# Kernel optimization log

Measured on AMD Instinct MI355X. Metric: run time of the kernel, lower is better.

## Reference

```python
import jax, jax.numpy as jnp
import numpy as np

EMBED_DIM = 1024
NUM_HEADS = 16
HEAD_DIM = EMBED_DIM // NUM_HEADS  # 64
B, T = 4, 2048
ROPE_BASE = 10000.0


def rope_tables(T, head_dim):
    # matches RotaryPositionalEmbedding: inv_freq over even indices
    inv_freq = 1.0 / (ROPE_BASE ** (jnp.arange(0, head_dim, 2, dtype=jnp.float32) / head_dim))
    freqs = jnp.arange(T, dtype=jnp.float32)[:, None] * inv_freq[None, :]  # [T, head_dim//2]
    emb = jnp.concatenate([freqs, freqs], axis=-1)  # [T, head_dim]
    return jnp.cos(emb), jnp.sin(emb)


def apply_rotary(x, cos, sin):
    # x: [B, H, T, D]; cos/sin: [T, D] but only first D//2 cols used (as in torch code)
    d = x.shape[-1] // 2
    x1, x2 = x[..., :d], x[..., d:]
    c = cos[None, None, :, :d]
    s = sin[None, None, :, :d]
    return jnp.concatenate([x1 * c - x2 * s, x1 * s + x2 * c], axis=-1)


def setup_inputs() -> dict:
    key = jax.random.key(0)
    k1, k2, k3, k4 = jax.random.split(key, 4)
    x = jax.random.normal(k1, (B, T, EMBED_DIM), dtype=jnp.float32)
    attention_mask = jnp.ones((B, T), dtype=jnp.int32)
    W_qkv = jax.random.normal(k2, (EMBED_DIM, 3 * EMBED_DIM), dtype=jnp.float32) / np.sqrt(EMBED_DIM)
    W_out = jax.random.normal(k3, (EMBED_DIM, EMBED_DIM), dtype=jnp.float32) / np.sqrt(EMBED_DIM)
    b_out = jax.random.normal(k4, (EMBED_DIM,), dtype=jnp.float32) * 0.01
    return {"x": x, "attention_mask": attention_mask, "W_qkv": W_qkv, "W_out": W_out, "b_out": b_out}


def reference(x, attention_mask, W_qkv, W_out, b_out):
    Bq, Tq, C = x.shape
    H, D = NUM_HEADS, HEAD_DIM
    qkv = (x @ W_qkv).reshape(Bq, Tq, 3, H, D)
    qkv = jnp.transpose(qkv, (2, 0, 3, 1, 4))  # [3, B, H, T, D]
    q, k, v = qkv[0], qkv[1], qkv[2]

    cos, sin = rope_tables(Tq, D)
    q = apply_rotary(q, cos, sin)
    k = apply_rotary(k, cos, sin)

    scale = 1.0 / np.sqrt(D)
    attn = jnp.einsum('bhtd,bhsd->bhts', q, k) * scale  # [B, H, T, T]
    causal = jnp.tril(jnp.ones((Tq, Tq), dtype=bool))
    attn = jnp.where(causal[None, None], attn, -jnp.inf)
    pad = attention_mask[:, None, None, :] != 0  # [B,1,1,T]
    attn = jnp.where(pad, attn, -jnp.inf)
    attn = jax.nn.softmax(attn, axis=-1)
    out = jnp.einsum('bhts,bhsd->bthd', attn, v).reshape(Bq, Tq, C)
    return out @ W_out + b_out
```

## Files before the change

### kernel.cpp

```cpp
#include <hip/hip_runtime.h>
#include <hip/hip_bf16.h>
#include <math.h>

typedef __attribute__((ext_vector_type(8))) __bf16 bf16x8;
typedef __attribute__((ext_vector_type(4))) __bf16 bf16x4;
typedef __attribute__((ext_vector_type(4))) float f32x4;

#define B_ 4
#define T_ 2048
#define C_ 1024
#define H_ 16
#define D_ 64
#define M_TOT (B_*T_)

static __device__ __forceinline__ f32x4 mfma_bf16(bf16x8 a, bf16x8 b, f32x4 c) {
  return __builtin_amdgcn_mfma_f32_16x16x32_bf16(a, b, c, 0, 0, 0);
}

static __device__ __forceinline__ void gload_lds16(const void* g, void* l) {
  __builtin_amdgcn_global_load_lds((const __attribute__((address_space(1))) void*)g,
                                   (__attribute__((address_space(3))) void*)l, 16, 0, 0);
}

__global__ void prep_cvt_rope(const float* __restrict__ in, __bf16* __restrict__ out,
                              float* __restrict__ cosT, float* __restrict__ sinT) {
  const int bid = blockIdx.x;
  if (bid < 8192) {
    int i = bid * 256 + threadIdx.x;
    float4 v = ((const float4*)in)[i];
    bf16x4 o = { (__bf16)v.x, (__bf16)v.y, (__bf16)v.z, (__bf16)v.w };
    *(bf16x4*)(out + (size_t)i*4) = o;
  } else {
    int idx = (bid - 8192) * 256 + threadIdx.x;
    int t = idx >> 5, d = idx & 31;
    float inv = powf(10000.0f, -((float)(2*d)) / 64.0f);
    float ang = (float)t * inv;
    cosT[idx] = cosf(ang);
    sinT[idx] = sinf(ang);
  }
}

__global__ void prep_transpose(const float* __restrict__ Wqkv, __bf16* __restrict__ wqkvT,
                               const float* __restrict__ Wout, __bf16* __restrict__ woutT) {
  __shared__ float tile[32][33];
  const int bx = blockIdx.x;
  const float* in;  __bf16* out;  int N, n0;
  if (bx < 96) { in = Wqkv; out = wqkvT; N = 3072; n0 = bx * 32; }
  else         { in = Wout; out = woutT; N = 1024; n0 = (bx - 96) * 32; }
  const int K = 1024;
  int k0 = blockIdx.y * 32;
  int tx = threadIdx.x & 31, ty = threadIdx.x >> 5;
  #pragma unroll
  for (int r = ty; r < 32; r += 8) tile[r][tx] = in[(size_t)(k0 + r)*N + n0 + tx];
  __syncthreads();
  #pragma unroll
  for (int r = ty; r < 32; r += 8) out[(size_t)(n0 + r)*K + k0 + tx] = (__bf16)tile[tx][r];
}

__global__ void __launch_bounds__(256)
vtrans_k(const __bf16* __restrict__ v, __bf16* __restrict__ vt) {
  __shared__ __bf16 tile[64][72];
  const int tid = threadIdx.x;
  const int bh = blockIdx.y;
  const int t0 = blockIdx.x * 64;
  const __bf16* src = v + ((size_t)bh*T_ + t0)*D_;
  #pragma unroll
  for (int c = 0; c < 2; ++c) {
    int idx = tid + c*256;
    int row = idx >> 3, col8 = (idx & 7) * 8;
    *(bf16x8*)&tile[row][col8] = *(const bf16x8*)(src + row*D_ + col8);
  }
  __syncthreads();
  __bf16* dst = vt + (size_t)bh*D_*T_ + t0;
  #pragma unroll
  for (int c = 0; c < 2; ++c) {
    int idx = tid + c*256;
    int d = idx >> 3, t8 = (idx & 7) * 8;
    bf16x8 ov;
    #pragma unroll
    for (int j = 0; j < 8; ++j) ov[j] = tile[t8 + j][d];
    *(bf16x8*)(dst + (size_t)d*T_ + t8) = ov;
  }
}


#define GEMM_PHASES(N_TILES)                                                     \
  auto RD_BFR = [&](const char* lb, bf16x8 (*bfr)[2]) {                          \
    _Pragma("unroll")                                                            \
    for (int n = 0; n < 4; ++n) {                                                \
      const int row = wc*64 + n*16 + l15;                                        \
      const int sw = (row & 7) << 4;                                             \
      _Pragma("unroll")                                                          \
      for (int ks = 0; ks < 2; ++ks)                                             \
        bfr[n][ks] = *(const bf16x8*)(lb + row*128 + ((ks*64 + lhi*16) ^ sw));   \
    }                                                                            \
  };                                                                             \
  auto RD_AF = [&](const char* la, int mb, bf16x8 (*af)[2]) {                    \
    _Pragma("unroll")                                                            \
    for (int mm = 0; mm < 2; ++mm) {                                             \
      const int row = wr*64 + (mb + mm)*16 + l15;                                \
      const int sw = (row & 7) << 4;                                             \
      _Pragma("unroll")                                                          \
      for (int ks = 0; ks < 2; ++ks)                                             \
        af[mm][ks] = *(const bf16x8*)(la + row*128 + ((ks*64 + lhi*16) ^ sw));   \
    }                                                                            \
  };                                                                             \
  auto MFMA16 = [&](bf16x8 (*af)[2], bf16x8 (*bfr)[2], int mb) {                 \
    __builtin_amdgcn_s_setprio(1);                                               \
    _Pragma("unroll")                                                            \
    for (int mm = 0; mm < 2; ++mm)                                               \
      _Pragma("unroll")                                                          \
      for (int n = 0; n < 4; ++n)                                                \
        _Pragma("unroll")                                                        \
        for (int ks = 0; ks < 2; ++ks)                                           \
          acc[mb + mm][n] = mfma_bf16(af[mm][ks], bfr[n][ks], acc[mb + mm][n]);  \
    __builtin_amdgcn_s_setprio(0);                                               \
  };                                                                             \
  STAGE_B(0, (char*)lB[0]); STAGE_A(0, (char*)lA[0]); STAGE_B(1, (char*)lB[1]);  \
  asm volatile("s_waitcnt vmcnt(4)" ::: "memory");                               \
  __builtin_amdgcn_s_barrier();                                                  \
  _Pragma("unroll")                                                              \
  for (int it = 0; it < (N_TILES)/2; ++it) {                                     \
    const int t0 = it*2;                                                         \
    bf16x8 bfr[4][2], af[2][2];                                                  \
    RD_BFR((const char*)lB[0], bfr);                                             \
    RD_AF((const char*)lA[0], 0, af);                                            \
    STAGE_A(t0 + 1, (char*)lA[1]);                                               \
    __builtin_amdgcn_s_barrier();                                                \
    MFMA16(af, bfr, 0);                                                          \
    __builtin_amdgcn_s_barrier();                                                \
    RD_AF((const char*)lA[0], 2, af);                                            \
    if (t0 + 2 < (N_TILES)) STAGE_B(t0 + 2, (char*)lB[0]);                       \
    __builtin_amdgcn_s_barrier();                                                \
    MFMA16(af, bfr, 2);                                                          \
    if (t0 + 2 < (N_TILES)) asm volatile("s_waitcnt vmcnt(4)" ::: "memory");     \
    else                    asm volatile("s_waitcnt vmcnt(0)" ::: "memory");     \
    __builtin_amdgcn_s_barrier();                                                \
    RD_BFR((const char*)lB[1], bfr);                                             \
    RD_AF((const char*)lA[1], 0, af);                                            \
    if (t0 + 2 < (N_TILES)) STAGE_A(t0 + 2, (char*)lA[0]);                       \
    __builtin_amdgcn_s_barrier();                                                \
    MFMA16(af, bfr, 0);                                                          \
    __builtin_amdgcn_s_barrier();                                                \
    RD_AF((const char*)lA[1], 2, af);                                            \
    if (t0 + 3 < (N_TILES)) STAGE_B(t0 + 3, (char*)lB[1]);                       \
    __builtin_amdgcn_s_barrier();                                                \
    MFMA16(af, bfr, 2);                                                          \
    if (it < (N_TILES)/2 - 1) asm volatile("s_waitcnt vmcnt(4)" ::: "memory");   \
    __builtin_amdgcn_s_barrier();                                                \
  }

__global__ void __launch_bounds__(512, 2)
gemm_qkv_p(const __bf16* __restrict__ A, const __bf16* __restrict__ Bt,
           __bf16* __restrict__ qout, __bf16* __restrict__ kout, __bf16* __restrict__ vout,
           const float* __restrict__ cosT, const float* __restrict__ sinT)
{
  __shared__ __attribute__((aligned(16))) __bf16 lA[2][128*64];
  __shared__ __attribute__((aligned(16))) __bf16 lB[2][256*64];
  const int tid = threadIdx.x;
  const int lane = tid & 63, wave = tid >> 6;
  const int wr = wave >> 2, wc = wave & 3;
  const int l15 = lane & 15, lhi = lane >> 4;

  const int id = blockIdx.x;
  const int xcd = id & 7, j = id >> 3;
  const int rowt = xcd*8 + (j & 7);
  const int row0 = rowt * 128;
  const int col0 = (j >> 3) * 256;

  f32x4 acc[4][4] = {};

  const char* Abase = (const char*)A + (size_t)row0 * 2048;
  const char* Bbase = (const char*)Bt + (size_t)col0 * 2048;

  auto STAGE_A = [&](int kt, char* dst) {
    #pragma unroll
    for (int c = 0; c < 2; ++c) {
      const int L = tid*16 + c*8192;
      const int row = L >> 7, colb = L & 127;
      const int sb = colb ^ ((row & 7) << 4);
      gload_lds16(Abase + (size_t)row*2048 + kt*128 + sb, dst + L);
    }
  };
  auto STAGE_B = [&](int kt, char* dst) {
    #pragma unroll
    for (int c = 0; c < 4; ++c) {
      const int L = tid*16 + c*8192;
      const int row = L >> 7, colb = L & 127;
      const int sb = colb ^ ((row & 7) << 4);
      gload_lds16(Bbase + (size_t)row*2048 + kt*128 + sb, dst + L);
    }
  };

  GEMM_PHASES(16)

  const int slot = (col0 >> 6) + wc;
  const int which = slot >> 4;
  const int h = slot & 15;
  const float fsc = (which == 0) ? 0.18033688011112042f : 1.0f;
  #pragma unroll
  for (int m = 0; m < 4; ++m) {
    #pragma unroll
    for (int r = 0; r < 4; ++r) {
      const int grow = row0 + wr*64 + m*16 + lhi*4 + r;
      const int b = grow >> 11, t = grow & 2047;
      const size_t obase = ((size_t)(b*H_ + h)*T_ + t)*D_;
      if (which == 2) {
        #pragma unroll
        for (int n = 0; n < 4; ++n)
          vout[obase + n*16 + l15] = (__bf16)acc[m][n][r];
      } else {
        __bf16* dst = (which == 0) ? qout : kout;
        #pragma unroll
        for (int n = 0; n < 2; ++n) {
          const int d1 = n*16 + l15;
          const float c = cosT[t*32 + d1];
          const float s = sinT[t*32 + d1];
          const float x1 = acc[m][n][r];
          const float x2 = acc[m][n+2][r];
          dst[obase + d1]      = (__bf16)((x1*c - x2*s) * fsc);
          dst[obase + d1 + 32] = (__bf16)((x1*s + x2*c) * fsc);
        }
      }
    }
  }
}

__global__ void __launch_bounds__(512, 2)
gemm_out_p(const __bf16* __restrict__ A, const __bf16* __restrict__ Bt,
           float* __restrict__ fout, const float* __restrict__ bias)
{
  __shared__ __attribute__((aligned(16))) __bf16 lA[2][128*64];
  __shared__ __attribute__((aligned(16))) __bf16 lB[2][256*64];
  const int tid = threadIdx.x;
  const int lane = tid & 63, wave = tid >> 6;
  const int wr = wave >> 2, wc = wave & 3;
  const int l15 = lane & 15, lhi = lane >> 4;

  const int id = blockIdx.x;
  const int xcd = id & 7, j = id >> 3;
  const int rowt = xcd*8 + (j & 7);
  const int row0 = rowt * 128;
  const int col0 = (j >> 3) * 256;

  f32x4 acc[4][4] = {};

  const char* Abase = (const char*)A + (size_t)row0 * 2048;
  const char* Bbase = (const char*)Bt + (size_t)col0 * 2048;

  auto STAGE_A = [&](int kt, char* dst) {
    #pragma unroll
    for (int c = 0; c < 2; ++c) {
      const int L = tid*16 + c*8192;
      const int row = L >> 7, colb = L & 127;
      const int sb = colb ^ ((row & 7) << 4);
      gload_lds16(Abase + (size_t)row*2048 + kt*128 + sb, dst + L);
    }
  };
  auto STAGE_B = [&](int kt, char* dst) {
    #pragma unroll
    for (int c = 0; c < 4; ++c) {
      const int L = tid*16 + c*8192;
      const int row = L >> 7, colb = L & 127;
      const int sb = colb ^ ((row & 7) << 4);
      gload_lds16(Bbase + (size_t)row*2048 + kt*128 + sb, dst + L);
    }
  };

  GEMM_PHASES(16)

  #pragma unroll
  for (int m = 0; m < 4; ++m) {
    #pragma unroll
    for (int r = 0; r < 4; ++r) {
      const int grow = row0 + wr*64 + m*16 + lhi*4 + r;
      #pragma unroll
      for (int n = 0; n < 4; ++n) {
        const int gcol = col0 + wc*64 + n*16 + l15;
        fout[(size_t)grow*1024 + gcol] = acc[m][n][r] + bias[gcol];
      }
    }
  }
}

#define THR_LOG2 8.0f

static __device__ const char QB_TAB[24] = {15,15,7,14,14,13,13,6,12,12,11,11,5,10,10,9,9,4,8,8,3,2,1,0};
static __device__ const char SP_TAB[24] = { 0, 1,2, 0, 1, 0, 1,2, 0, 1, 0, 1,2, 0, 1,0,1,2,0,1,2,2,2,2};

__global__ void __launch_bounds__(256, 3)
attn_kernel(const __bf16* __restrict__ q, const __bf16* __restrict__ k,
            const __bf16* __restrict__ vt, const int* __restrict__ amask,
            __bf16* __restrict__ aout,
            float* __restrict__ pO, float* __restrict__ pM, float* __restrict__ pL)
{
  __shared__ __attribute__((aligned(16))) __bf16 lK[64*64];
  __shared__ __attribute__((aligned(16))) __bf16 lVt[64*64];
  __shared__ __attribute__((aligned(16))) __bf16 lP[4][32*64];
  __shared__ __attribute__((aligned(16))) __bf16 lQ[128*64];
  const int tid = threadIdx.x;
  const int lane = tid & 63, wave = tid >> 6;
  const int l15 = lane & 15, lhi = lane >> 4;

  const int g = blockIdx.x >> 6;
  const int bh = blockIdx.x & 63;
  const int qblock = QB_TAB[g];
  const int sp = SP_TAB[g];
  const int kb0   = (sp == 1) ? (qblock + 1) : 0;
  const int kbend = (sp == 0) ? (qblock + 1) : (2*qblock + 2);

  const int b = bh >> 4, h = bh & 15;
  const size_t kvbase = (size_t)bh * T_ * D_;
  const char* kbase  = (const char*)(k + kvbase);
  const char* vtbase = (const char*)(vt + kvbase);
  char* lPw = (char*)lP[wave];

  const int q0w = qblock*128 + wave*32;

  {
    const char* qgbase = (const char*)(q + kvbase) + (size_t)qblock*128*128;
    #pragma unroll
    for (int c = 0; c < 4; ++c) {
      const int L = tid*16 + c*4096;
      const int row = L >> 7;
      const int sb = (L & 127) ^ ((row & 7) << 4);
      gload_lds16(qgbase + (size_t)row*128 + sb, (char*)lQ + L);
    }
  }

  f32x4 acc_o[2][4] = {};
  f32x4 acc_l[2] = {};
  float m_w = -3e37f;

  for (int kb = kb0; kb < kbend; ++kb) {
    #pragma unroll
    for (int c = 0; c < 2; ++c) {
      const int L = tid*16 + c*4096;
      const int row = L >> 7;
      const int sb  = (L & 127) ^ ((row & 7) << 4);
      gload_lds16(kbase  + (size_t)(kb*64 + row)*128 + sb, (char*)lK + L);
      gload_lds16(vtbase + (size_t)row*(T_*2) + (size_t)kb*128 + sb, (char*)lVt + L);
    }
    __syncthreads();

    if (kb*64 <= q0w + 31) {
      const char* lKc = (const char*)lK;
      const char* lVc = (const char*)lVt;
      const char* lQw = (const char*)lQ + (wave*32)*128;
      asm volatile("" : "+v"(lQw));

      bf16x8 aq[2][2];
      #pragma unroll
      for (int m = 0; m < 2; ++m) {
        const int lr = m*16 + l15;
        const int sw = (lr & 7) << 4;
        #pragma unroll
        for (int ks = 0; ks < 2; ++ks)
          aq[m][ks] = *(const bf16x8*)(lQw + lr*128 + ((ks*64 + lhi*16) ^ sw));
      }

      f32x4 sc[2][4] = {};
      __builtin_amdgcn_s_setprio(1);
      #pragma unroll
      for (int n = 0; n < 4; ++n) {
        const int row = n*16 + l15;
        const int sw = (row & 7) << 4;
        #pragma unroll
        for (int ks = 0; ks < 2; ++ks) {
          bf16x8 bk = *(const bf16x8*)(lKc + row*128 + ((ks*64 + lhi*16) ^ sw));
          #pragma unroll
          for (int m = 0; m < 2; ++m)
            sc[m][n] = mfma_bf16(aq[m][ks], bk, sc[m][n]);
        }
      }
      __builtin_amdgcn_s_setprio(0);

      if (kb*64 + 63 > q0w) {
        #pragma unroll
        for (int m = 0; m < 2; ++m)
          #pragma unroll
          for (int r = 0; r < 4; ++r) {
            const int tq = q0w + m*16 + lhi*4 + r;
            #pragma unroll
            for (int n = 0; n < 4; ++n)
              if (kb*64 + n*16 + l15 > tq) sc[m][n][r] = -3e37f;
          }
      }

      f32x4 vm = sc[0][0];
      #pragma unroll
      for (int m = 0; m < 2; ++m)
        #pragma unroll
        for (int n = 0; n < 4; ++n) {
          if (m == 0 && n == 0) continue;
          #pragma unroll
          for (int r = 0; r < 4; ++r) vm[r] = fmaxf(vm[r], sc[m][n][r]);
        }
      float tmax = fmaxf(fmaxf(vm[0], vm[1]), fmaxf(vm[2], vm[3]));
      #pragma unroll
      for (int off = 1; off < 64; off <<= 1)
        tmax = fmaxf(tmax, __shfl_xor(tmax, off));

      if (tmax > m_w + THR_LOG2) {
        const float corr = __builtin_amdgcn_exp2f(m_w - tmax);
        #pragma unroll
        for (int m = 0; m < 2; ++m) {
          #pragma unroll
          for (int c = 0; c < 4; ++c) acc_o[m][c] *= corr;
          acc_l[m] *= corr;
        }
        m_w = tmax;
      }

      float mk[4];
      #pragma unroll
      for (int n = 0; n < 4; ++n)
        mk[n] = (amask[b*T_ + kb*64 + n*16 + l15] != 0) ? m_w : 3e37f;

      #pragma unroll
      for (int m = 0; m < 2; ++m)
        #pragma unroll
        for (int r = 0; r < 4; ++r) {
          const int row = m*16 + lhi*4 + r;
          const int sw = (row & 7) << 4;
          #pragma unroll
          for (int n = 0; n < 4; ++n) {
            const float p = __builtin_amdgcn_exp2f(sc[m][n][r] - mk[n]);
            *(__bf16*)(lPw + row*128 + ((((n*16 + l15)*2)) ^ sw)) = (__bf16)p;
          }
        }

      bf16x8 pa[2][2];
      #pragma unroll
      for (int m = 0; m < 2; ++m) {
        const int row = m*16 + l15;
        const int sw = (row & 7) << 4;
        #pragma unroll
        for (int ks = 0; ks < 2; ++ks)
          pa[m][ks] = *(const bf16x8*)(lPw + row*128 + ((ks*64 + lhi*16) ^ sw));
      }

      __builtin_amdgcn_s_setprio(1);
      const __bf16 one = (__bf16)1.0f;
      const bf16x8 vone = {one, one, one, one, one, one, one, one};
      #pragma unroll
      for (int m = 0; m < 2; ++m)
        #pragma unroll
        for (int ks = 0; ks < 2; ++ks)
          acc_l[m] = mfma_bf16(pa[m][ks], vone, acc_l[m]);

      #pragma unroll
      for (int c = 0; c < 4; ++c) {
        const int row = c*16 + l15;
        const int sw = (row & 7) << 4;
        #pragma unroll
        for (int ks = 0; ks < 2; ++ks) {
          bf16x8 bv = *(const bf16x8*)(lVc + row*128 + ((ks*64 + lhi*16) ^ sw));
          #pragma unroll
          for (int m = 0; m < 2; ++m)
            acc_o[m][c] = mfma_bf16(pa[m][ks], bv, acc_o[m][c]);
        }
      }
      __builtin_amdgcn_s_setprio(0);
    }
    __syncthreads();
  }

  if (sp == 2) {
    #pragma unroll
    for (int m = 0; m < 2; ++m)
      #pragma unroll
      for (int r = 0; r < 4; ++r) {
        const int tq = q0w + m*16 + lhi*4 + r;
        const float invl = 1.0f / acc_l[m][r];
        const size_t obase = ((size_t)b*T_ + tq)*C_ + h*D_;
        #pragma unroll
        for (int c = 0; c < 4; ++c)
          aout[obase + c*16 + l15] = (__bf16)(acc_o[m][c][r] * invl);
      }
  } else {
    const int pidx = ((qblock - 8)*2 + sp)*64 + bh;
    float* po = pO + (size_t)pidx*128*64;
    float* pm = pM + pidx*128;
    float* pl = pL + pidx*128;
    #pragma unroll
    for (int m = 0; m < 2; ++m)
      #pragma unroll
      for (int r = 0; r < 4; ++r) {
        const int rw = wave*32 + m*16 + lhi*4 + r;
        if (l15 == 0) { pm[rw] = m_w; pl[rw] = acc_l[m][r]; }
        #pragma unroll
        for (int c = 0; c < 4; ++c)
          po[(size_t)rw*64 + c*16 + l15] = acc_o[m][c][r];
      }
  }
}

__global__ void __launch_bounds__(256)
attn_combine(const float* __restrict__ pO, const float* __restrict__ pM,
             const float* __restrict__ pL, __bf16* __restrict__ aout)
{
  const int g = blockIdx.x;
  const int qb8 = g >> 6, bh = g & 63;
  const int p0 = (qb8*2)*64 + bh, p1 = (qb8*2 + 1)*64 + bh;
  const int row = threadIdx.x >> 1, ch = threadIdx.x & 1;
  const float m0 = pM[p0*128 + row], m1 = pM[p1*128 + row];
  const float l0 = pL[p0*128 + row], l1 = pL[p1*128 + row];
  const float M = fmaxf(m0, m1);
  const float w0 = __builtin_amdgcn_exp2f(m0 - M);
  const float w1 = __builtin_amdgcn_exp2f(m1 - M);
  const float inv = 1.0f / (l0*w0 + l1*w1);
  const int b = bh >> 4, h = bh & 15;
  const int t = (qb8 + 8)*128 + row;
  const float* o0 = pO + ((size_t)p0*128 + row)*64 + ch*32;
  const float* o1 = pO + ((size_t)p1*128 + row)*64 + ch*32;
  __bf16* dst = aout + ((size_t)b*T_ + t)*C_ + h*D_ + ch*32;
  #pragma unroll
  for (int j = 0; j < 32; j += 4) {
    float4 a = *(const float4*)(o0 + j);
    float4 c = *(const float4*)(o1 + j);
    bf16x4 rr;
    rr[0] = (__bf16)((a.x*w0 + c.x*w1) * inv);
    rr[1] = (__bf16)((a.y*w0 + c.y*w1) * inv);
    rr[2] = (__bf16)((a.z*w0 + c.z*w1) * inv);
    rr[3] = (__bf16)((a.w*w0 + c.w*w1) * inv);
    *(bf16x4*)(dst + j) = rr;
  }
}


extern "C" void kernel_launch(void* const* d_in, const int* in_sizes, int n_in,
                              void* d_out, int out_size, void* d_ws, size_t ws_size,
                              hipStream_t stream)
{
  const float* x     = (const float*)d_in[0];
  const int*   amask = (const int*)d_in[1];
  const float* Wqkv  = (const float*)d_in[2];
  const float* Wout  = (const float*)d_in[3];
  const float* bout  = (const float*)d_in[4];
  float* out = (float*)d_out;

  char* w = (char*)d_ws;
  __bf16* xb    = (__bf16*)w;  w += (size_t)M_TOT*C_*2;
  __bf16* wqkvT = (__bf16*)w;  w += (size_t)3072*1024*2;
  __bf16* woutT = (__bf16*)w;  w += (size_t)1024*1024*2;
  __bf16* qb    = (__bf16*)w;  w += (size_t)B_*H_*T_*D_*2;
  __bf16* kb    = (__bf16*)w;  w += (size_t)B_*H_*T_*D_*2;
  __bf16* vb    = (__bf16*)w;  w += (size_t)B_*H_*T_*D_*2;
  __bf16* aob   = (__bf16*)w;  w += (size_t)M_TOT*C_*2;
  float*  cosT  = (float*)w;   w += (size_t)T_*32*4;
  float*  sinT  = (float*)w;   w += (size_t)T_*32*4;
  float*  pO    = (float*)w;   w += (size_t)1024*128*64*4;
  float*  pM    = (float*)w;   w += (size_t)1024*128*4;
  float*  pL    = (float*)w;   w += (size_t)1024*128*4;
  __bf16* vtb   = xb;

  prep_cvt_rope<<<dim3(8192 + 256), 256, 0, stream>>>(x, xb, cosT, sinT);
  prep_transpose<<<dim3(128, 32), 256, 0, stream>>>(Wqkv, wqkvT, Wout, woutT);

  gemm_qkv_p<<<dim3(768), 512, 0, stream>>>(xb, wqkvT, qb, kb, vb, cosT, sinT);

  vtrans_k<<<dim3(T_/64, B_*H_), 256, 0, stream>>>(vb, vtb);

  attn_kernel<<<dim3(1536), 256, 0, stream>>>(qb, kb, vtb, amask, aob, pO, pM, pL);
  attn_combine<<<dim3(512), 256, 0, stream>>>(pO, pM, pL, aob);

  gemm_out_p<<<dim3(256), 512, 0, stream>>>(aob, woutT, out, bout);
}
```

Baseline: 201.2 us.

## Fuse prep kernels and write transposed V directly from QKV GEMM epilogue

Merges the activation conversion, rope table and weight transpose kernels into one launch, and moves the V transpose into the QKV GEMM epilogue by staging each wave's 64x64 V tile through LDS and writing it out in [D,T] layout. This removes two kernel launches plus one full read and write of V. In exchange, the GEMM's shared memory is reorganised into a single buffer that the epilogue reuses, and the V write path adds per-wave LDS traffic.

```diff
diff --git a/kernel.cpp b/kernel.cpp
--- a/kernel.cpp
+++ b/kernel.cpp
@@ -22,64 +22,35 @@
                                    (__attribute__((address_space(3))) void*)l, 16, 0, 0);
 }
 
-__global__ void prep_cvt_rope(const float* __restrict__ in, __bf16* __restrict__ out,
-                              float* __restrict__ cosT, float* __restrict__ sinT) {
+__global__ void prep_all(const float* __restrict__ x, __bf16* __restrict__ xb,
+                         float* __restrict__ cosT, float* __restrict__ sinT,
+                         const float* __restrict__ Wqkv, __bf16* __restrict__ wqkvT,
+                         const float* __restrict__ Wout, __bf16* __restrict__ woutT) {
+  __shared__ float tile[32][33];
   const int bid = blockIdx.x;
   if (bid < 8192) {
     int i = bid * 256 + threadIdx.x;
-    float4 v = ((const float4*)in)[i];
+    float4 v = ((const float4*)x)[i];
     bf16x4 o = { (__bf16)v.x, (__bf16)v.y, (__bf16)v.z, (__bf16)v.w };
-    *(bf16x4*)(out + (size_t)i*4) = o;
-  } else {
+    *(bf16x4*)(xb + (size_t)i*4) = o;
+  } else if (bid < 8448) {
     int idx = (bid - 8192) * 256 + threadIdx.x;
     int t = idx >> 5, d = idx & 31;
     float inv = powf(10000.0f, -((float)(2*d)) / 64.0f);
     float ang = (float)t * inv;
     cosT[idx] = cosf(ang);
     sinT[idx] = sinf(ang);
-  }
-}
-
-__global__ void prep_transpose(const float* __restrict__ Wqkv, __bf16* __restrict__ wqkvT,
-                               const float* __restrict__ Wout, __bf16* __restrict__ woutT) {
-  __shared__ float tile[32][33];
-  const int bx = blockIdx.x;
-  const float* in;  __bf16* out;  int N, n0;
-  if (bx < 96) { in = Wqkv; out = wqkvT; N = 3072; n0 = bx * 32; }
-  else         { in = Wout; out = woutT; N = 1024; n0 = (bx - 96) * 32; }
-  const int K = 1024;
-  int k0 = blockIdx.y * 32;
-  int tx = threadIdx.x & 31, ty = threadIdx.x >> 5;
-  #pragma unroll
-  for (int r = ty; r < 32; r += 8) tile[r][tx] = in[(size_t)(k0 + r)*N + n0 + tx];
-  __syncthreads();
-  #pragma unroll
-  for (int r = ty; r < 32; r += 8) out[(size_t)(n0 + r)*K + k0 + tx] = (__bf16)tile[tx][r];
-}
-
-__global__ void __launch_bounds__(256)
-vtrans_k(const __bf16* __restrict__ v, __bf16* __restrict__ vt) {
-  __shared__ __bf16 tile[64][72];
-  const int tid = threadIdx.x;
-  const int bh = blockIdx.y;
-  const int t0 = blockIdx.x * 64;
-  const __bf16* src = v + ((size_t)bh*T_ + t0)*D_;
-  #pragma unroll
-  for (int c = 0; c < 2; ++c) {
-    int idx = tid + c*256;
-    int row = idx >> 3, col8 = (idx & 7) * 8;
-    *(bf16x8*)&tile[row][col8] = *(const bf16x8*)(src + row*D_ + col8);
-  }
-  __syncthreads();
-  __bf16* dst = vt + (size_t)bh*D_*T_ + t0;
-  #pragma unroll
-  for (int c = 0; c < 2; ++c) {
-    int idx = tid + c*256;
-    int d = idx >> 3, t8 = (idx & 7) * 8;
-    bf16x8 ov;
-    #pragma unroll
-    for (int j = 0; j < 8; ++j) ov[j] = tile[t8 + j][d];
-    *(bf16x8*)(dst + (size_t)d*T_ + t8) = ov;
+  } else {
+    int tId = bid - 8448;
+    const float* in;  __bf16* out;  int N, n0, k0;
+    if (tId < 3072) { in = Wqkv; out = wqkvT; N = 3072; n0 = (tId % 96)*32; k0 = (tId / 96)*32; }
+    else { tId -= 3072; in = Wout; out = woutT; N = 1024; n0 = (tId % 32)*32; k0 = (tId / 32)*32; }
+    int tx = threadIdx.x & 31, ty = threadIdx.x >> 5;
+    #pragma unroll
+    for (int r = ty; r < 32; r += 8) tile[r][tx] = in[(size_t)(k0 + r)*N + n0 + tx];
+    __syncthreads();
+    #pragma unroll
+    for (int r = ty; r < 32; r += 8) out[(size_t)(n0 + r)*1024 + k0 + tx] = (__bf16)tile[tx][r];
   }
 }
 
@@ -152,11 +123,12 @@
 
 __global__ void __launch_bounds__(512, 2)
 gemm_qkv_p(const __bf16* __restrict__ A, const __bf16* __restrict__ Bt,
-           __bf16* __restrict__ qout, __bf16* __restrict__ kout, __bf16* __restrict__ vout,
+           __bf16* __restrict__ qout, __bf16* __restrict__ kout, __bf16* __restrict__ vtout,
            const float* __restrict__ cosT, const float* __restrict__ sinT)
 {
-  __shared__ __attribute__((aligned(16))) __bf16 lA[2][128*64];
-  __shared__ __attribute__((aligned(16))) __bf16 lB[2][256*64];
+  __shared__ __attribute__((aligned(16))) char smem[98304];
+  auto lA = (__bf16 (*)[128*64])smem;
+  auto lB = (__bf16 (*)[256*64])(smem + 32768);
   const int tid = threadIdx.x;
   const int lane = tid & 63, wave = tid >> 6;
   const int wr = wave >> 2, wc = wave & 3;
@@ -197,20 +169,39 @@
   const int slot = (col0 >> 6) + wc;
   const int which = slot >> 4;
   const int h = slot & 15;
-  const float fsc = (which == 0) ? 0.18033688011112042f : 1.0f;
-  #pragma unroll
-  for (int m = 0; m < 4; ++m) {
-    #pragma unroll
-    for (int r = 0; r < 4; ++r) {
-      const int grow = row0 + wr*64 + m*16 + lhi*4 + r;
-      const int b = grow >> 11, t = grow & 2047;
-      const size_t obase = ((size_t)(b*H_ + h)*T_ + t)*D_;
-      if (which == 2) {
+  if (which == 2) {
+    __bf16* lTw = (__bf16*)(smem + wave*9216);
+    #pragma unroll
+    for (int m = 0; m < 4; ++m)
+      #pragma unroll
+      for (int r = 0; r < 4; ++r) {
+        const int trow = m*16 + lhi*4 + r;
         #pragma unroll
         for (int n = 0; n < 4; ++n)
-          vout[obase + n*16 + l15] = (__bf16)acc[m][n][r];
-      } else {
-        __bf16* dst = (which == 0) ? qout : kout;
+          lTw[trow*72 + n*16 + l15] = (__bf16)acc[m][n][r];
+      }
+    const int t0w = row0 + wr*64;
+    const int b = t0w >> 11, tloc = t0w & 2047;
+    __bf16* dstv = vtout + ((size_t)(b*H_ + h)*D_)*T_;
+    #pragma unroll
+    for (int c2 = 0; c2 < 8; ++c2) {
+      const int idx = lane + c2*64;
+      const int d = idx >> 3, t8 = (idx & 7)*8;
+      bf16x8 ov;
+      #pragma unroll
+      for (int jj = 0; jj < 8; ++jj) ov[jj] = lTw[(t8 + jj)*72 + d];
+      *(bf16x8*)(dstv + (size_t)d*T_ + tloc + t8) = ov;
+    }
+  } else {
+    __bf16* dst = (which == 0) ? qout : kout;
+    const float fsc = (which == 0) ? 0.18033688011112042f : 1.0f;
+    #pragma unroll
+    for (int m = 0; m < 4; ++m) {
+      #pragma unroll
+      for (int r = 0; r < 4; ++r) {
+        const int grow = row0 + wr*64 + m*16 + lhi*4 + r;
+        const int b = grow >> 11, t = grow & 2047;
+        const size_t obase = ((size_t)(b*H_ + h)*T_ + t)*D_;
         #pragma unroll
         for (int n = 0; n < 2; ++n) {
           const int d1 = n*16 + l15;
@@ -546,21 +537,18 @@
   __bf16* woutT = (__bf16*)w;  w += (size_t)1024*1024*2;
   __bf16* qb    = (__bf16*)w;  w += (size_t)B_*H_*T_*D_*2;
   __bf16* kb    = (__bf16*)w;  w += (size_t)B_*H_*T_*D_*2;
-  __bf16* vb    = (__bf16*)w;  w += (size_t)B_*H_*T_*D_*2;
+  __bf16* vtb   = (__bf16*)w;  w += (size_t)B_*H_*T_*D_*2;
   __bf16* aob   = (__bf16*)w;  w += (size_t)M_TOT*C_*2;
   float*  cosT  = (float*)w;   w += (size_t)T_*32*4;
   float*  sinT  = (float*)w;   w += (size_t)T_*32*4;
   float*  pO    = (float*)w;   w += (size_t)1024*128*64*4;
   float*  pM    = (float*)w;   w += (size_t)1024*128*4;
   float*  pL    = (float*)w;   w += (size_t)1024*128*4;
-  __bf16* vtb   = xb;
-
-  prep_cvt_rope<<<dim3(8192 + 256), 256, 0, stream>>>(x, xb, cosT, sinT);
-  prep_transpose<<<dim3(128, 32), 256, 0, stream>>>(Wqkv, wqkvT, Wout, woutT);
-
-  gemm_qkv_p<<<dim3(768), 512, 0, stream>>>(xb, wqkvT, qb, kb, vb, cosT, sinT);
-
-  vtrans_k<<<dim3(T_/64, B_*H_), 256, 0, stream>>>(vb, vtb);
+
+  prep_all<<<dim3(8192 + 256 + 3072 + 1024), 256, 0, stream>>>(
+      x, xb, cosT, sinT, Wqkv, wqkvT, Wout, woutT);
+
+  gemm_qkv_p<<<dim3(768), 512, 0, stream>>>(xb, wqkvT, qb, kb, vtb, cosT, sinT);
 
   attn_kernel<<<dim3(1536), 256, 0, stream>>>(qb, kb, vtb, amask, aob, pO, pM, pL);
   attn_combine<<<dim3(512), 256, 0, stream>>>(pO, pM, pL, aob);
```

After: 182.4 us. -9.4%, faster.
